# Kernel optimization log

Hardware: AMD Instinct MI355X
Metric: run time of the kernel (lower is better)

## Reference

```python
import jax, jax.numpy as jnp
import numpy as np

N = 100000        # num_nodes
E_HALF = 800000   # directed edges; full symmetric edge list has 2*E_HALF
D = 64            # feature dim (hard-coded Linear(64,64) in source)
STEP = 1.0        # step_size


def setup_inputs() -> dict:
    key = jax.random.key(0)
    k1, k2, k3, k4, k5, k6 = jax.random.split(key, 6)
    src = jax.random.randint(k1, (E_HALF,), 0, N)
    dst = jax.random.randint(k2, (E_HALF,), 0, N)
    # symmetric edge list: edge e in [0,E_HALF) has its reverse at e+E_HALF
    edge_index = jnp.stack([jnp.concatenate([src, dst]),
                            jnp.concatenate([dst, src])])  # (2, 2*E_HALF)
    left_idx = jnp.arange(2 * E_HALF)
    right_idx = jnp.concatenate([jnp.arange(E_HALF, 2 * E_HALF),
                                 jnp.arange(0, E_HALF)])
    x = jax.random.normal(k3, (N, D), dtype=jnp.float32)
    W_sheaf = jax.random.normal(k4, (1, 2 * D), dtype=jnp.float32) * 0.08  # sheaf_learner (128->1, no bias)
    W_lin = jax.random.normal(k5, (D, D), dtype=jnp.float32) * 0.125       # linear 64->64
    b_lin = jax.random.normal(k6, (D,), dtype=jnp.float32) * 0.01
    return {"x": x, "W_sheaf": W_sheaf, "W_lin": W_lin, "b_lin": b_lin,
            "edge_index": edge_index, "left_idx": left_idx, "right_idx": right_idx}


def reference(x, W_sheaf, W_lin, b_lin, edge_index, left_idx, right_idx):
    row, col = edge_index[0], edge_index[1]
    # predict_restriction_maps: gather endpoints, concat, linear, tanh -> (E,1)
    x_row = x[row]
    x_col = x[col]
    maps = jnp.tanh(jnp.concatenate([x_row, x_col], axis=1) @ W_sheaf.T)  # (E,1)
    # build_laplacian
    left_maps = maps[left_idx]
    right_maps = maps[right_idx]
    non_diag_maps = -left_maps * right_maps                                # (E,1)
    diag_maps = jax.ops.segment_sum(maps ** 2, row, num_segments=N)       # (N,1)
    d_sqrt_inv = jax.lax.rsqrt(diag_maps + 1.0)                            # (N,1)
    norm_maps = d_sqrt_inv[row] * non_diag_maps * d_sqrt_inv[col]          # (E,1)
    diag = d_sqrt_inv * diag_maps * d_sqrt_inv                             # (N,1)
    # y = linear(x); sparse Laplacian @ y = diag part + scatter-add of edge part
    y = x @ W_lin.T + b_lin                                                # (N,D)
    Ly = diag * y + jax.ops.segment_sum(norm_maps * y[col], row, num_segments=N)
    return x - STEP * Ly
```

## Files before the change

kernel.cpp:

```cpp
#include <hip/hip_runtime.h>
#include <hip/hip_fp16.h>


#define NBLK_BIN 256

__global__ __launch_bounds__(256) void k_node_pre(
    const float* __restrict__ x,
    const float* __restrict__ Wsheaf,
    const float* __restrict__ Wlin,
    const float* __restrict__ blin,
    float2* __restrict__ s12,
    __half* __restrict__ yh,
    int N)
{
    __shared__ float4 xt[64 * 16];

    int tid  = threadIdx.x;
    int lane = tid & 63;
    int wave = tid >> 6;
    int n0   = blockIdx.x * 64;

    float wreg[64];
    {
        const float4* Wv = (const float4*)(Wlin + lane * 64);
        #pragma unroll
        for (int q = 0; q < 16; ++q) {
            float4 w4 = Wv[q];
            wreg[4 * q + 0] = w4.x; wreg[4 * q + 1] = w4.y;
            wreg[4 * q + 2] = w4.z; wreg[4 * q + 3] = w4.w;
        }
    }
    float bl  = blin[lane];
    float ws1 = Wsheaf[lane];
    float ws2 = Wsheaf[64 + lane];

    int nvalid = min(64, N - n0);
    const float4* xg = (const float4*)(x + (size_t)n0 * 64);
    for (int i = tid; i < nvalid * 16; i += 256) xt[i] = xg[i];
    __syncthreads();

    int ni_end = min(wave * 16 + 16, nvalid);
    for (int ni = wave * 16; ni < ni_end; ++ni) {
        float xv = ((const float*)xt)[ni * 64 + lane];
        float a = xv * ws1, b = xv * ws2;
        #pragma unroll
        for (int m = 32; m; m >>= 1) {
            a += __shfl_xor(a, m);
            b += __shfl_xor(b, m);
        }
        if (lane == 0) s12[n0 + ni] = make_float2(a, b);

        float acc = bl;
        #pragma unroll
        for (int q = 0; q < 16; ++q) {
            float4 xq = xt[ni * 16 + q];
            acc += xq.x * wreg[4 * q + 0] + xq.y * wreg[4 * q + 1]
                 + xq.z * wreg[4 * q + 2] + xq.w * wreg[4 * q + 3];
        }
        yh[(size_t)(n0 + ni) * 64 + lane] = __float2half(acc);
    }
}

__global__ __launch_bounds__(256) void k_hist(
    const int* __restrict__ row, const int* __restrict__ col,
    unsigned* __restrict__ table, int Eh, int NB)
{
    __shared__ unsigned h[512];
    int tid = threadIdx.x;
    for (int i = tid; i < NB; i += 256) h[i] = 0;
    __syncthreads();
    int chunk = (Eh + NBLK_BIN - 1) / NBLK_BIN;
    int lo = blockIdx.x * chunk, hi = min(lo + chunk, Eh);
    for (int i = lo + tid; i < hi; i += 256) {
        atomicAdd(&h[(unsigned)row[i] >> 8], 1u);
        atomicAdd(&h[(unsigned)col[i] >> 8], 1u);
    }
    __syncthreads();
    for (int i = tid; i < NB; i += 256) table[(size_t)blockIdx.x * NB + i] = h[i];
}

__global__ __launch_bounds__(256) void k_colscan(
    unsigned* __restrict__ table, unsigned* __restrict__ colsum, int NB)
{
    __shared__ unsigned sm[256];
    int j = blockIdx.x, t = threadIdx.x;
    unsigned v = table[(size_t)t * NB + j];
    sm[t] = v;
    __syncthreads();
    for (int off = 1; off < 256; off <<= 1) {
        unsigned u = (t >= off) ? sm[t - off] : 0;
        __syncthreads();
        if (t >= off) sm[t] += u;
        __syncthreads();
    }
    table[(size_t)t * NB + j] = sm[t] - v;
    if (t == 255) colsum[j] = sm[255];
}

__global__ __launch_bounds__(512) void k_ebase(
    const unsigned* __restrict__ colsum, unsigned* __restrict__ ebase, int NB)
{
    __shared__ unsigned sm[512];
    int t = threadIdx.x;
    unsigned v = (t < NB) ? colsum[t] : 0;
    sm[t] = v;
    __syncthreads();
    for (int off = 1; off < 512; off <<= 1) {
        unsigned u = (t >= off) ? sm[t - off] : 0;
        __syncthreads();
        if (t >= off) sm[t] += u;
        __syncthreads();
    }
    if (t <= NB) ebase[t] = sm[t] - v;
}

__global__ __launch_bounds__(256) void k_binplace(
    const float2* __restrict__ s12,
    const int* __restrict__ row, const int* __restrict__ col,
    const unsigned* __restrict__ table, const unsigned* __restrict__ ebase,
    uint2* __restrict__ binned, int Eh, int NB)
{
    __shared__ unsigned destbase[512];
    __shared__ unsigned cur[512];
    int tid = threadIdx.x;
    for (int i = tid; i < NB; i += 256) {
        destbase[i] = ebase[i] + table[(size_t)blockIdx.x * NB + i];
        cur[i] = 0;
    }
    __syncthreads();
    int chunk = (Eh + NBLK_BIN - 1) / NBLK_BIN;
    int lo = blockIdx.x * chunk, hi = min(lo + chunk, Eh);
    for (int i = lo + tid; i < hi; i += 256) {
        int r = row[i], c = col[i];
        float2 sr = s12[r], sc2 = s12[c];
        float mf = tanhf(sr.x + sc2.y);
        float mr = tanhf(sc2.x + sr.y);
        float pr = mf * mr;

        __half2 h1 = __halves2half2(__float2half_rn(mf * mf), __float2half_rn(pr));
        unsigned u1 = *reinterpret_cast<unsigned*>(&h1);
        unsigned bk_r = (unsigned)r >> 8;
        unsigned d1 = destbase[bk_r] + atomicAdd(&cur[bk_r], 1u);
        binned[d1] = make_uint2(((unsigned)(r & 255) << 17) | (unsigned)c, u1);

        __half2 h2 = __halves2half2(__float2half_rn(mr * mr), __float2half_rn(pr));
        unsigned u2 = *reinterpret_cast<unsigned*>(&h2);
        unsigned bk_c = (unsigned)c >> 8;
        unsigned d2 = destbase[bk_c] + atomicAdd(&cur[bk_c], 1u);
        binned[d2] = make_uint2(((unsigned)(c & 255) << 17) | (unsigned)r, u2);
    }
}

__global__ __launch_bounds__(256) void k_bucket(
    const uint2* __restrict__ binned,
    const unsigned* __restrict__ ebase,
    int* __restrict__ base, float* __restrict__ dinv,
    int2* __restrict__ sc, int N, int NB)
{
    __shared__ unsigned cnt[256];
    __shared__ float dsum[256];
    __shared__ unsigned pref[256];
    __shared__ unsigned cur[256];

    int b = blockIdx.x, t = threadIdx.x;
    int row0 = b << 8;
    cnt[t] = 0;
    dsum[t] = 0.0f;
    __syncthreads();

    int lo = (int)ebase[b], hi = (int)ebase[b + 1];
    for (int i = lo + t; i < hi; i += 256) {
        uint2 v = binned[i];
        unsigned rl = v.x >> 17;
        atomicAdd(&cnt[rl], 1u);
        __half2 h = *reinterpret_cast<__half2*>(&v.y);
        atomicAdd(&dsum[rl], __low2float(h));
    }
    __syncthreads();

    unsigned myc = cnt[t];
    pref[t] = myc;
    __syncthreads();
    for (int off = 1; off < 256; off <<= 1) {
        unsigned u = (t >= off) ? pref[t - off] : 0;
        __syncthreads();
        if (t >= off) pref[t] += u;
        __syncthreads();
    }
    unsigned excl = pref[t] - myc;
    int rown = row0 + t;
    if (rown < N) {
        base[rown] = lo + (int)excl;
        dinv[rown] = rsqrtf(dsum[t] + 1.0f);
    }
    if (b == (int)gridDim.x - 1 && t == 0) base[N] = hi;
    cur[t] = excl;
    __syncthreads();

    for (int i = lo + t; i < hi; i += 256) {
        uint2 v = binned[i];
        unsigned rl = v.x >> 17;
        unsigned other = v.x & 0x1FFFFu;
        unsigned slot = (unsigned)lo + atomicAdd(&cur[rl], 1u);
        __half2 h = *reinterpret_cast<__half2*>(&v.y);
        sc[slot] = make_int2((int)other, __float_as_int(__high2float(h)));
    }
}

__global__ __launch_bounds__(256) void k_node_gather(
    const float* __restrict__ x,
    const __half* __restrict__ yh,
    const float* __restrict__ dinv,
    const int* __restrict__ base,
    const int2* __restrict__ sc,
    float* __restrict__ out,
    int N)
{
    int lane = threadIdx.x & 63;
    int n = blockIdx.x * 4 + (threadIdx.x >> 6);
    if (n >= N) return;
    int j = base[n];
    int end = base[n + 1];
    float acc = 0.0f;
    for (; j + 3 < end; j += 4) {
        int2 p0 = sc[j], p1 = sc[j + 1], p2 = sc[j + 2], p3 = sc[j + 3];
        acc += __int_as_float(p0.y) * dinv[p0.x] * __half2float(yh[(size_t)p0.x * 64 + lane])
             + __int_as_float(p1.y) * dinv[p1.x] * __half2float(yh[(size_t)p1.x * 64 + lane])
             + __int_as_float(p2.y) * dinv[p2.x] * __half2float(yh[(size_t)p2.x * 64 + lane])
             + __int_as_float(p3.y) * dinv[p3.x] * __half2float(yh[(size_t)p3.x * 64 + lane]);
    }
    for (; j < end; ++j) {
        int2 p = sc[j];
        acc += __int_as_float(p.y) * dinv[p.x] * __half2float(yh[(size_t)p.x * 64 + lane]);
    }
    float dv = dinv[n];
    float scale = 1.0f - dv * dv;
    int idx = n * 64 + lane;
    float yv = __half2float(yh[idx]);
    out[idx] = x[idx] - scale * yv + dv * acc;
}

extern "C" void kernel_launch(void* const* d_in, const int* in_sizes, int n_in,
                              void* d_out, int out_size, void* d_ws, size_t ws_size,
                              hipStream_t stream) {
    const float* x      = (const float*)d_in[0];
    const float* Wsheaf = (const float*)d_in[1];
    const float* Wlin   = (const float*)d_in[2];
    const float* blin   = (const float*)d_in[3];
    const int*   ei     = (const int*)d_in[4];
    float* out = (float*)d_out;

    int N  = in_sizes[0] / 64;
    int E  = in_sizes[4] / 2;
    int Eh = E >> 1;
    int NB = (N + 255) >> 8;
    const int* row = ei;
    const int* col = ei + E;

    char* ws = (char*)d_ws;
    float2*   s12    = (float2*)ws;             ws += (size_t)N * 8;
    uint2*    binned = (uint2*)ws;              ws += (size_t)E * 8;
    int2*     sc     = (int2*)ws;               ws += (size_t)E * 8;
    unsigned* table  = (unsigned*)ws;           ws += (size_t)NBLK_BIN * NB * 4;
    unsigned* colsum = (unsigned*)ws;           ws += (size_t)NB * 4;
    unsigned* ebase  = (unsigned*)ws;           ws += (size_t)(NB + 1) * 4;
    int*      base   = (int*)ws;                ws += (size_t)(N + 1) * 4;
    float*    dinv   = (float*)ws;              ws += (size_t)N * 4;
    __half*   yh     = (__half*)ws;             ws += (size_t)N * 64 * 2;

    k_node_pre <<<(N + 63) / 64, 256, 0, stream>>>(x, Wsheaf, Wlin, blin, s12, yh, N);
    k_hist     <<<NBLK_BIN, 256, 0, stream>>>(row, col, table, Eh, NB);
    k_colscan  <<<NB, 256, 0, stream>>>(table, colsum, NB);
    k_ebase    <<<1, 512, 0, stream>>>(colsum, ebase, NB);
    k_binplace <<<NBLK_BIN, 256, 0, stream>>>(s12, row, col, table, ebase, binned, Eh, NB);
    k_bucket   <<<NB, 256, 0, stream>>>(binned, ebase, base, dinv, sc, N, NB);
    k_node_gather<<<(N + 3) / 4, 256, 0, stream>>>(x, yh, dinv, base, sc, out, N);
}
```

Baseline: 268.6 us.

## Fuse node-pre with histogram, fold ebase scan, prescale y by dinv in bucket

Merges the node precompute and the edge histogram into one launch, and replaces the separate ebase scan kernel with scans done inside binplace (now 512 threads) and bucket. The bucket kernel also prescales y by dinv for its rows, so the gather no longer does a per-edge dinv lookup. The gather stages edge entries through shared memory per wave. Together these remove two launches and one random load per edge, at the cost of a redundant prefix scan in every block, an extra read-modify-write pass over y in half precision, and an extra rounding step.

```diff
diff --git a/kernel.cpp b/kernel.cpp
--- a/kernel.cpp
+++ b/kernel.cpp
@@ -4,18 +4,36 @@
 
 #define NBLK_BIN 256
 
-__global__ __launch_bounds__(256) void k_node_pre(
+__global__ __launch_bounds__(256) void k_pre_hist(
     const float* __restrict__ x,
     const float* __restrict__ Wsheaf,
     const float* __restrict__ Wlin,
     const float* __restrict__ blin,
     float2* __restrict__ s12,
-    __half* __restrict__ yh,
-    int N)
+    __half* __restrict__ yz,
+    const int* __restrict__ row, const int* __restrict__ col,
+    unsigned* __restrict__ table,
+    int N, int Eh, int NB, int NPRE)
 {
     __shared__ float4 xt[64 * 16];
-
-    int tid  = threadIdx.x;
+    int tid = threadIdx.x;
+
+    if (blockIdx.x >= NPRE) {
+        unsigned* h = (unsigned*)xt;
+        int hb = blockIdx.x - NPRE;
+        for (int i = tid; i < NB; i += 256) h[i] = 0;
+        __syncthreads();
+        int chunk = (Eh + NBLK_BIN - 1) / NBLK_BIN;
+        int lo = hb * chunk, hi = min(lo + chunk, Eh);
+        for (int i = lo + tid; i < hi; i += 256) {
+            atomicAdd(&h[(unsigned)row[i] >> 8], 1u);
+            atomicAdd(&h[(unsigned)col[i] >> 8], 1u);
+        }
+        __syncthreads();
+        for (int i = tid; i < NB; i += 256) table[(size_t)hb * NB + i] = h[i];
+        return;
+    }
+
     int lane = tid & 63;
     int wave = tid >> 6;
     int n0   = blockIdx.x * 64;
@@ -57,26 +75,8 @@
             acc += xq.x * wreg[4 * q + 0] + xq.y * wreg[4 * q + 1]
                  + xq.z * wreg[4 * q + 2] + xq.w * wreg[4 * q + 3];
         }
-        yh[(size_t)(n0 + ni) * 64 + lane] = __float2half(acc);
-    }
-}
-
-__global__ __launch_bounds__(256) void k_hist(
-    const int* __restrict__ row, const int* __restrict__ col,
-    unsigned* __restrict__ table, int Eh, int NB)
-{
-    __shared__ unsigned h[512];
-    int tid = threadIdx.x;
-    for (int i = tid; i < NB; i += 256) h[i] = 0;
-    __syncthreads();
-    int chunk = (Eh + NBLK_BIN - 1) / NBLK_BIN;
-    int lo = blockIdx.x * chunk, hi = min(lo + chunk, Eh);
-    for (int i = lo + tid; i < hi; i += 256) {
-        atomicAdd(&h[(unsigned)row[i] >> 8], 1u);
-        atomicAdd(&h[(unsigned)col[i] >> 8], 1u);
-    }
-    __syncthreads();
-    for (int i = tid; i < NB; i += 256) table[(size_t)blockIdx.x * NB + i] = h[i];
+        yz[(size_t)(n0 + ni) * 64 + lane] = __float2half(acc);
+    }
 }
 
 __global__ __launch_bounds__(256) void k_colscan(
@@ -97,40 +97,35 @@
     if (t == 255) colsum[j] = sm[255];
 }
 
-__global__ __launch_bounds__(512) void k_ebase(
-    const unsigned* __restrict__ colsum, unsigned* __restrict__ ebase, int NB)
-{
-    __shared__ unsigned sm[512];
-    int t = threadIdx.x;
-    unsigned v = (t < NB) ? colsum[t] : 0;
-    sm[t] = v;
-    __syncthreads();
-    for (int off = 1; off < 512; off <<= 1) {
-        unsigned u = (t >= off) ? sm[t - off] : 0;
-        __syncthreads();
-        if (t >= off) sm[t] += u;
-        __syncthreads();
-    }
-    if (t <= NB) ebase[t] = sm[t] - v;
-}
-
-__global__ __launch_bounds__(256) void k_binplace(
+__global__ __launch_bounds__(512) void k_binplace(
     const float2* __restrict__ s12,
     const int* __restrict__ row, const int* __restrict__ col,
-    const unsigned* __restrict__ table, const unsigned* __restrict__ ebase,
+    const unsigned* __restrict__ table, const unsigned* __restrict__ colsum,
     uint2* __restrict__ binned, int Eh, int NB)
 {
+    __shared__ unsigned csum[512];
     __shared__ unsigned destbase[512];
     __shared__ unsigned cur[512];
-    int tid = threadIdx.x;
-    for (int i = tid; i < NB; i += 256) {
-        destbase[i] = ebase[i] + table[(size_t)blockIdx.x * NB + i];
-        cur[i] = 0;
-    }
-    __syncthreads();
+    int t = threadIdx.x;
+
+    unsigned v = (t < NB) ? colsum[t] : 0;
+    csum[t] = v;
+    __syncthreads();
+    for (int off = 1; off < 512; off <<= 1) {
+        unsigned u = (t >= off) ? csum[t - off] : 0;
+        __syncthreads();
+        csum[t] += u;
+        __syncthreads();
+    }
+    if (t < NB) {
+        destbase[t] = (csum[t] - v) + table[(size_t)blockIdx.x * NB + t];
+        cur[t] = 0;
+    }
+    __syncthreads();
+
     int chunk = (Eh + NBLK_BIN - 1) / NBLK_BIN;
     int lo = blockIdx.x * chunk, hi = min(lo + chunk, Eh);
-    for (int i = lo + tid; i < hi; i += 256) {
+    for (int i = lo + t; i < hi; i += 512) {
         int r = row[i], c = col[i];
         float2 sr = s12[r], sc2 = s12[c];
         float mf = tanhf(sr.x + sc2.y);
@@ -153,22 +148,35 @@
 
 __global__ __launch_bounds__(256) void k_bucket(
     const uint2* __restrict__ binned,
-    const unsigned* __restrict__ ebase,
+    const unsigned* __restrict__ colsum,
     int* __restrict__ base, float* __restrict__ dinv,
-    int2* __restrict__ sc, int N, int NB)
+    int2* __restrict__ sc,
+    __half* __restrict__ yz,
+    int N, int NB)
 {
     __shared__ unsigned cnt[256];
     __shared__ float dsum[256];
     __shared__ unsigned pref[256];
     __shared__ unsigned cur[256];
+    __shared__ float sdinv[256];
+    __shared__ unsigned red[256];
 
     int b = blockIdx.x, t = threadIdx.x;
     int row0 = b << 8;
+
+    unsigned part = 0;
+    for (int j = t; j < b; j += 256) part += colsum[j];
+    red[t] = part;
     cnt[t] = 0;
     dsum[t] = 0.0f;
     __syncthreads();
-
-    int lo = (int)ebase[b], hi = (int)ebase[b + 1];
+    for (int m = 128; m; m >>= 1) {
+        if (t < m) red[t] += red[t + m];
+        __syncthreads();
+    }
+    int lo = (int)red[0];
+    int hi = lo + (int)colsum[b];
+
     for (int i = lo + t; i < hi; i += 256) {
         uint2 v = binned[i];
         unsigned rl = v.x >> 17;
@@ -188,10 +196,12 @@
         __syncthreads();
     }
     unsigned excl = pref[t] - myc;
+    float dv = rsqrtf(dsum[t] + 1.0f);
+    sdinv[t] = dv;
     int rown = row0 + t;
     if (rown < N) {
         base[rown] = lo + (int)excl;
-        dinv[rown] = rsqrtf(dsum[t] + 1.0f);
+        dinv[rown] = dv;
     }
     if (b == (int)gridDim.x - 1 && t == 0) base[N] = hi;
     cur[t] = excl;
@@ -205,39 +215,47 @@
         __half2 h = *reinterpret_cast<__half2*>(&v.y);
         sc[slot] = make_int2((int)other, __float_as_int(__high2float(h)));
     }
+
+    for (int i = t; i < 256 * 64; i += 256) {
+        int rl = i >> 6;
+        int rn = row0 + rl;
+        if (rn < N) {
+            size_t idx = (size_t)rn * 64 + (i & 63);
+            yz[idx] = __float2half(sdinv[rl] * __half2float(yz[idx]));
+        }
+    }
 }
 
 __global__ __launch_bounds__(256) void k_node_gather(
     const float* __restrict__ x,
-    const __half* __restrict__ yh,
+    const __half* __restrict__ zh,
     const float* __restrict__ dinv,
     const int* __restrict__ base,
     const int2* __restrict__ sc,
     float* __restrict__ out,
     int N)
 {
+    __shared__ int2 stage[4][64];
     int lane = threadIdx.x & 63;
-    int n = blockIdx.x * 4 + (threadIdx.x >> 6);
+    int wave = threadIdx.x >> 6;
+    int n = blockIdx.x * 4 + wave;
     if (n >= N) return;
-    int j = base[n];
-    int end = base[n + 1];
+
+    int j0 = base[n], end = base[n + 1];
     float acc = 0.0f;
-    for (; j + 3 < end; j += 4) {
-        int2 p0 = sc[j], p1 = sc[j + 1], p2 = sc[j + 2], p3 = sc[j + 3];
-        acc += __int_as_float(p0.y) * dinv[p0.x] * __half2float(yh[(size_t)p0.x * 64 + lane])
-             + __int_as_float(p1.y) * dinv[p1.x] * __half2float(yh[(size_t)p1.x * 64 + lane])
-             + __int_as_float(p2.y) * dinv[p2.x] * __half2float(yh[(size_t)p2.x * 64 + lane])
-             + __int_as_float(p3.y) * dinv[p3.x] * __half2float(yh[(size_t)p3.x * 64 + lane]);
-    }
-    for (; j < end; ++j) {
-        int2 p = sc[j];
-        acc += __int_as_float(p.y) * dinv[p.x] * __half2float(yh[(size_t)p.x * 64 + lane]);
+    for (int blk = j0; blk < end; blk += 64) {
+        int m = min(64, end - blk);
+        if (lane < m) stage[wave][lane] = sc[blk + lane];
+        #pragma unroll 4
+        for (int j = 0; j < m; ++j) {
+            int2 r = stage[wave][j];
+            acc += __int_as_float(r.y) * __half2float(zh[(size_t)r.x * 64 + lane]);
+        }
     }
     float dv = dinv[n];
-    float scale = 1.0f - dv * dv;
     int idx = n * 64 + lane;
-    float yv = __half2float(yh[idx]);
-    out[idx] = x[idx] - scale * yv + dv * acc;
+    float zv = __half2float(zh[idx]);
+    out[idx] = x[idx] - (1.0f / dv - dv) * zv + dv * acc;
 }
 
 extern "C" void kernel_launch(void* const* d_in, const int* in_sizes, int n_in,
@@ -254,6 +272,7 @@
     int E  = in_sizes[4] / 2;
     int Eh = E >> 1;
     int NB = (N + 255) >> 8;
+    int NPRE = (N + 63) / 64;
     const int* row = ei;
     const int* col = ei + E;
 
@@ -263,16 +282,14 @@
     int2*     sc     = (int2*)ws;               ws += (size_t)E * 8;
     unsigned* table  = (unsigned*)ws;           ws += (size_t)NBLK_BIN * NB * 4;
     unsigned* colsum = (unsigned*)ws;           ws += (size_t)NB * 4;
-    unsigned* ebase  = (unsigned*)ws;           ws += (size_t)(NB + 1) * 4;
     int*      base   = (int*)ws;                ws += (size_t)(N + 1) * 4;
     float*    dinv   = (float*)ws;              ws += (size_t)N * 4;
-    __half*   yh     = (__half*)ws;             ws += (size_t)N * 64 * 2;
-
-    k_node_pre <<<(N + 63) / 64, 256, 0, stream>>>(x, Wsheaf, Wlin, blin, s12, yh, N);
-    k_hist     <<<NBLK_BIN, 256, 0, stream>>>(row, col, table, Eh, NB);
+    __half*   yz     = (__half*)ws;             ws += (size_t)N * 64 * 2;
+
+    k_pre_hist <<<NPRE + NBLK_BIN, 256, 0, stream>>>(x, Wsheaf, Wlin, blin, s12, yz,
+                                                     row, col, table, N, Eh, NB, NPRE);
     k_colscan  <<<NB, 256, 0, stream>>>(table, colsum, NB);
-    k_ebase    <<<1, 512, 0, stream>>>(colsum, ebase, NB);
-    k_binplace <<<NBLK_BIN, 256, 0, stream>>>(s12, row, col, table, ebase, binned, Eh, NB);
-    k_bucket   <<<NB, 256, 0, stream>>>(binned, ebase, base, dinv, sc, N, NB);
-    k_node_gather<<<(N + 3) / 4, 256, 0, stream>>>(x, yh, dinv, base, sc, out, N);
-}
+    k_binplace <<<NBLK_BIN, 512, 0, stream>>>(s12, row, col, table, colsum, binned, Eh, NB);
+    k_bucket   <<<NB, 256, 0, stream>>>(binned, colsum, base, dinv, sc, yz, N, NB);
+    k_node_gather<<<(N + 3) / 4, 256, 0, stream>>>(x, yz, dinv, base, sc, out, N);
+}
```

Result: faster. 256.8 us (-4.4%).
